# Kernel tuning notes

Hardware: AMD Instinct MI355X
Metric: run time of the kernel (lower is better)

## Reference

```python
import jax, jax.numpy as jnp
import numpy as np

E = 8          # num_experts
K = 2          # top-k experts per token
CAP_RATIO = 1.05


def setup_inputs() -> dict:
    key = jax.random.key(0)
    ks = jax.random.split(key, 4)
    B, S, D, H = 2, 2048, 1024, 4096
    x = jax.random.normal(ks[0], (B, S, D), jnp.float32)
    Wg = jax.random.normal(ks[1], (E, D), jnp.float32) * 0.02
    W1 = jax.random.normal(ks[2], (E, D, H), jnp.float32) * 0.02
    b1 = jnp.zeros((E, H), jnp.float32)
    W2 = jax.random.normal(ks[3], (E, H, D), jnp.float32) * 0.02
    b2 = jnp.zeros((E, D), jnp.float32)
    return {"x": x, "Wg": Wg, "W1": W1, "b1": b1, "W2": W2, "b2": b2}


def reference(x, Wg, W1, b1, W2, b2):
    # Eval-mode SparseMoE forward (no router noise, no aux-loss metrics).
    B, S, D = x.shape
    T = B * S
    xf = x.reshape(T, D)

    # --- router: softmax gates + top-k ---
    gates = jax.nn.softmax(xf @ Wg.T, axis=-1)          # [T, E]
    topw, topi = jax.lax.top_k(gates, K)                # [T, K]

    # --- capacity-limited dispatch (slot-major order, matching torch loop) ---
    C = int(round(K * T * CAP_RATIO / E))               # buffer capacity per expert
    e_ord = topi.T.reshape(-1)                          # [K*T] expert id per assignment
    tok_ord = jnp.tile(jnp.arange(T), K)                # [K*T] token id per assignment
    oh = jax.nn.one_hot(e_ord, E, dtype=jnp.int32)      # [K*T, E]
    cnt = jnp.take_along_axis(jnp.cumsum(oh, 0) - oh, e_ord[:, None], 1)[:, 0]
    within = cnt < C                                    # first C arrivals per expert accepted
    pos = jnp.where(within, cnt, C)                     # dropped tokens -> dummy slot C

    # scatter accepted tokens into per-expert buffers [E, C+1, D]
    x_disp = xf[tok_ord]
    buf = jnp.zeros((E, C + 1, D), xf.dtype).at[e_ord, pos].add(x_disp)[:, :C]

    # --- grouped expert MLP (Linear -> exact GELU -> Linear) ---
    h = jax.nn.gelu(jnp.einsum('ecd,edh->ech', buf, W1) + b1[:, None, :],
                    approximate=False)
    y = jnp.einsum('ech,ehd->ecd', h, W2) + b2[:, None, :]  # [E, C, D]

    # --- gather back and weighted combine ---
    y_ord = y[e_ord, jnp.minimum(pos, C - 1)] * within[:, None].astype(y.dtype)
    y_tk = y_ord.reshape(K, T, D).transpose(1, 0, 2)     # [T, K, D]
    cw = topw * within.reshape(K, T).T.astype(topw.dtype)
    out = jnp.einsum('tk,tkd->td', cw, y_tk)
    return out.reshape(B, S, D)
```

## Files before the change

kernel.cpp:

```cpp
#include <hip/hip_runtime.h>

typedef __attribute__((ext_vector_type(8))) __bf16 bf16x8;
typedef __attribute__((ext_vector_type(4))) float f32x4;

constexpr int T  = 4096;
constexpr int Dm = 1024;
constexpr int Hm = 4096;
constexpr int NE = 8;
constexpr int CAP = 1075;
constexpr int CP  = 1152;

static __device__ __forceinline__ unsigned short f2bf(float f) {
  unsigned int u = __float_as_uint(f);
  u += 0x7FFFu + ((u >> 16) & 1u);
  return (unsigned short)(u >> 16);
}

static __device__ __forceinline__ void gload_lds16(const void* g, void* l) {
  __builtin_amdgcn_global_load_lds(
      (const __attribute__((address_space(1))) void*)g,
      (__attribute__((address_space(3))) void*)l, 16, 0, 0);
}


static __device__ __forceinline__ void transpose_body(
    float (*tile)[33], const float* __restrict__ W, unsigned short* __restrict__ Wt,
    int Kd, int N, int e, int n0, int k0) {
  const float* src = W + ((long long)e * Kd + k0) * N + n0;
  const int tid = threadIdx.x;
  const int r = tid >> 3;
  const int c4 = (tid & 7) * 4;
#pragma unroll
  for (int hh = 0; hh < 2; ++hh) {
    float4 v = *(const float4*)(src + (long long)(r + 32 * hh) * N + c4);
    tile[r + 32 * hh][c4] = v.x; tile[r + 32 * hh][c4 + 1] = v.y;
    tile[r + 32 * hh][c4 + 2] = v.z; tile[r + 32 * hh][c4 + 3] = v.w;
  }
  __syncthreads();
  const int n = tid >> 4;
  const int k4 = (tid & 15) * 4;
  unsigned short* dst = Wt + ((long long)e * N + n0) * Kd + k0;
#pragma unroll
  for (int hh = 0; hh < 2; ++hh) {
    int nn = n + 16 * hh;
    ushort4 o;
    o.x = f2bf(tile[k4][nn]);     o.y = f2bf(tile[k4 + 1][nn]);
    o.z = f2bf(tile[k4 + 2][nn]); o.w = f2bf(tile[k4 + 3][nn]);
    *(ushort4*)(dst + (long long)nn * Kd + k4) = o;
  }
}

static __device__ __forceinline__ void router_body(
    const float* __restrict__ x, const float* __restrict__ Wg,
    int* __restrict__ topi, float* __restrict__ topw, int blk) {
  int t = blk * 4 + (threadIdx.x >> 6);
  int lane = threadIdx.x & 63;
  const float* xr = x + (size_t)t * Dm;
  float acc[NE];
#pragma unroll
  for (int e = 0; e < NE; ++e) acc[e] = 0.f;
  for (int i = lane * 4; i < Dm; i += 256) {
    float4 xv = *(const float4*)(xr + i);
#pragma unroll
    for (int e = 0; e < NE; ++e) {
      float4 wv = *(const float4*)(Wg + e * Dm + i);
      acc[e] += xv.x * wv.x + xv.y * wv.y + xv.z * wv.z + xv.w * wv.w;
    }
  }
#pragma unroll
  for (int off = 32; off > 0; off >>= 1) {
#pragma unroll
    for (int e = 0; e < NE; ++e) acc[e] += __shfl_xor(acc[e], off, 64);
  }
  if (lane == 0) {
    float mx = acc[0];
#pragma unroll
    for (int e = 1; e < NE; ++e) mx = fmaxf(mx, acc[e]);
    float g[NE];
    float s = 0.f;
#pragma unroll
    for (int e = 0; e < NE; ++e) { g[e] = expf(acc[e] - mx); s += g[e]; }
    int i0 = 0; float v0 = g[0];
#pragma unroll
    for (int e = 1; e < NE; ++e) if (g[e] > v0) { v0 = g[e]; i0 = e; }
    int i1 = -1; float v1 = -1e30f;
#pragma unroll
    for (int e = 0; e < NE; ++e) {
      if (e == i0) continue;
      if (g[e] > v1) { v1 = g[e]; i1 = e; }
    }
    float inv = 1.f / s;
    topi[t * 2] = i0; topi[t * 2 + 1] = i1;
    topw[t * 2] = v0 * inv; topw[t * 2 + 1] = v1 * inv;
  }
}

template <bool GELU, bool OUT_BF16>
static __device__ __forceinline__ void gemm_body(
    unsigned short* Alds, unsigned short* Blds,
    const unsigned short* __restrict__ A, const unsigned short* __restrict__ Bt,
    const float* __restrict__ bias, void* __restrict__ Out,
    int Kd, int N, int mb, int nb) {
  const unsigned short* Ab  = A  + (long long)mb * 128 * Kd;
  const unsigned short* Btb = Bt + (long long)nb * 128 * Kd;

  const int tid = threadIdx.x;
  const int lane = tid & 63;
  const int wid = tid >> 6;
  const int wr = (wid >> 1) * 64;
  const int wc = (wid & 1) * 64;
  const int l15 = lane & 15;
  const int khi = lane >> 4;
  const int swz = lane & 7;
  const int srow = lane >> 3;
  const int sslot = (lane & 7) ^ srow;

  f32x4 acc[4][4];
#pragma unroll
  for (int m = 0; m < 4; ++m)
#pragma unroll
    for (int n = 0; n < 4; ++n) acc[m][n] = (f32x4){0.f, 0.f, 0.f, 0.f};

  const int nK = Kd >> 6;
  for (int kt = 0; kt < nK; ++kt) {
    const int kb = kt << 6;
#pragma unroll
    for (int j = 0; j < 4; ++j) {
      const int c = wid * 4 + j;
      const long long rowg = 8 * c + srow;
      gload_lds16(Ab  + rowg * Kd + kb + sslot * 8, &Alds[c * 512]);
      gload_lds16(Btb + rowg * Kd + kb + sslot * 8, &Blds[c * 512]);
    }
    __syncthreads();
#pragma unroll
    for (int kk = 0; kk < 2; ++kk) {
      bf16x8 af[4], bfv[4];
#pragma unroll
      for (int m = 0; m < 4; ++m)
        af[m] = *(const bf16x8*)&Alds[(wr + m * 16 + l15) * 64 + (((kk * 4 + khi) ^ swz) << 3)];
#pragma unroll
      for (int n = 0; n < 4; ++n)
        bfv[n] = *(const bf16x8*)&Blds[(wc + n * 16 + l15) * 64 + (((kk * 4 + khi) ^ swz) << 3)];
#pragma unroll
      for (int m = 0; m < 4; ++m)
#pragma unroll
        for (int n = 0; n < 4; ++n)
          acc[m][n] = __builtin_amdgcn_mfma_f32_16x16x32_bf16(af[m], bfv[n], acc[m][n], 0, 0, 0);
    }
    __syncthreads();
  }

  const int crow = khi * 4;
#pragma unroll
  for (int m = 0; m < 4; ++m) {
#pragma unroll
    for (int n = 0; n < 4; ++n) {
      const long long col = (long long)nb * 128 + wc + n * 16 + l15;
      const float bvv = bias[nb * 128 + wc + n * 16 + l15];
#pragma unroll
      for (int j = 0; j < 4; ++j) {
        const long long row = (long long)mb * 128 + wr + m * 16 + crow + j;
        float v = acc[m][n][j] + bvv;
        if (GELU) v = 0.5f * v * (1.f + erff(v * 0.70710678118654752f));
        if (OUT_BF16)
          ((unsigned short*)Out)[row * N + col] = f2bf(v);
        else
          ((float*)Out)[row * N + col] = v;
      }
    }
  }
}


__global__ __launch_bounds__(256) void fused_pre_kernel(
    const float* __restrict__ x, const float* __restrict__ Wg,
    int* __restrict__ topi, float* __restrict__ topw,
    const float* __restrict__ W1, unsigned short* __restrict__ W1t,
    const float* __restrict__ W2, unsigned short* __restrict__ W2t,
    int nR, int nT) {
  __shared__ __align__(16) float tile[64][33];
  const int bid = blockIdx.x;
  if (bid < nR) {
    router_body(x, Wg, topi, topw, bid);
  } else if (bid < nR + nT) {
    int tb = bid - nR;
    int nb = tb % (Hm / 32);
    int rest = tb / (Hm / 32);
    int kb = rest % (Dm / 64);
    int e = rest / (Dm / 64);
    transpose_body(tile, W1, W1t, Dm, Hm, e, nb * 32, kb * 64);
  } else {
    int tb = bid - nR - nT;
    int nb = tb % (Dm / 32);
    int rest = tb / (Dm / 32);
    int kb = rest % (Hm / 64);
    int e = rest / (Hm / 64);
    transpose_body(tile, W2, W2t, Hm, Dm, e, nb * 32, kb * 64);
  }
}

__global__ __launch_bounds__(256) void transpose_kernel(
    const float* __restrict__ W, unsigned short* __restrict__ Wt, int Kd, int N) {
  __shared__ __align__(16) float tile[64][33];
  transpose_body(tile, W, Wt, Kd, N, blockIdx.z, blockIdx.x * 32, blockIdx.y * 64);
}

__global__ __launch_bounds__(1024) void dispatch_scan_kernel(
    const int* __restrict__ topi, int* __restrict__ pos, int* __restrict__ within) {
  __shared__ unsigned long long sc0[1024];
  __shared__ unsigned long long sc1[1024];
  const int tid = threadIdx.x;
  int myE[8];
  unsigned long long w0 = 0, w1 = 0;
#pragma unroll
  for (int j = 0; j < 8; ++j) {
    int a = tid * 8 + j;
    int k = a >> 12;
    int t = a & (T - 1);
    int e = topi[t * 2 + k];
    myE[j] = e;
    unsigned long long inc = 1ULL << (16 * (e & 3));
    if (e < 4) w0 += inc; else w1 += inc;
  }
  const unsigned long long l0 = w0, l1 = w1;
  sc0[tid] = w0; sc1[tid] = w1;
  __syncthreads();
  for (int off = 1; off < 1024; off <<= 1) {
    unsigned long long a0 = 0, a1 = 0;
    if (tid >= off) { a0 = sc0[tid - off]; a1 = sc1[tid - off]; }
    __syncthreads();
    w0 += a0; w1 += a1;
    sc0[tid] = w0; sc1[tid] = w1;
    __syncthreads();
  }
  unsigned long long e0 = w0 - l0, e1 = w1 - l1;
#pragma unroll
  for (int j = 0; j < 8; ++j) {
    int a = tid * 8 + j;
    int e = myE[j];
    int sh = 16 * (e & 3);
    int p;
    if (e < 4) { p = (int)((e0 >> sh) & 0xFFFF); e0 += 1ULL << sh; }
    else       { p = (int)((e1 >> sh) & 0xFFFF); e1 += 1ULL << sh; }
    pos[a] = p;
    within[a] = (p < CAP) ? 1 : 0;
  }
}

__global__ __launch_bounds__(256) void scatter_kernel(
    const float* __restrict__ x, const int* __restrict__ topi,
    const int* __restrict__ pos, const int* __restrict__ within,
    unsigned short* __restrict__ buf) {
  int a = blockIdx.x;
  if (!within[a]) return;
  int k = a >> 12, t = a & (T - 1);
  int e = topi[t * 2 + k];
  int p = pos[a];
  const float* src = x + (size_t)t * Dm;
  unsigned short* dst = buf + ((size_t)e * CP + p) * Dm;
  int i = threadIdx.x * 4;
  float4 v = *(const float4*)(src + i);
  ushort4 o;
  o.x = f2bf(v.x); o.y = f2bf(v.y); o.z = f2bf(v.z); o.w = f2bf(v.w);
  *(ushort4*)(dst + i) = o;
}

template <bool GELU, bool OUT_BF16>
__global__ __launch_bounds__(256) void gemm_bt_kernel(
    const unsigned short* __restrict__ Aall, const unsigned short* __restrict__ Btall,
    const float* __restrict__ biasAll, void* __restrict__ OutAll,
    int Kd, int N, long long sA, long long sB, long long sO, int sBias,
    int eb, int nM) {
  __shared__ __align__(16) char smem[32768];
  unsigned short* Alds = (unsigned short*)smem;
  unsigned short* Blds = (unsigned short*)(smem + 16384);
  const int lin = blockIdx.x;
  const int e = lin % eb;
  const int q = lin / eb;
  const int mb = q % nM;
  const int nb = q / nM;
  char* Out = (char*)OutAll + (long long)e * sO * (OUT_BF16 ? 2 : 4);
  gemm_body<GELU, OUT_BF16>(Alds, Blds,
      Aall + (long long)e * sA, Btall + (long long)e * sB,
      biasAll + (long long)e * sBias, (void*)Out, Kd, N, mb, nb);
}

__global__ __launch_bounds__(256) void combine_kernel(
    const float* __restrict__ y, const int* __restrict__ topi,
    const float* __restrict__ topw, const int* __restrict__ pos,
    const int* __restrict__ within, float* __restrict__ out) {
  int t = blockIdx.x;
  int i = threadIdx.x * 4;
  float4 r = {0.f, 0.f, 0.f, 0.f};
#pragma unroll
  for (int k = 0; k < 2; ++k) {
    int a = k * T + t;
    if (within[a]) {
      int e = topi[t * 2 + k];
      int p = pos[a];
      float w = topw[t * 2 + k];
      const float* yr = y + ((size_t)e * CP + p) * Dm;
      float4 v = *(const float4*)(yr + i);
      r.x += w * v.x; r.y += w * v.y; r.z += w * v.z; r.w += w * v.w;
    }
  }
  *(float4*)(out + (size_t)t * Dm + i) = r;
}

extern "C" void kernel_launch(void* const* d_in, const int* in_sizes, int n_in,
                              void* d_out, int out_size, void* d_ws, size_t ws_size,
                              hipStream_t stream) {
  const float* x  = (const float*)d_in[0];
  const float* Wg = (const float*)d_in[1];
  const float* W1 = (const float*)d_in[2];
  const float* b1 = (const float*)d_in[3];
  const float* W2 = (const float*)d_in[4];
  const float* b2 = (const float*)d_in[5];
  float* out = (float*)d_out;

  char* ws = (char*)d_ws;
  const size_t sz_h = (size_t)NE * CP * Hm * 2;
  const size_t sz_y = (size_t)NE * CP * Dm * 4;
  const size_t sz_w = (size_t)NE * Hm * Dm * 2;
  const size_t sz_small = (size_t)2 * T * 16;
  const size_t need_full = sz_h + sz_y + 2 * sz_w + sz_small;
  const size_t need_mid  = sz_h + sz_y + sz_w + sz_small;

  unsigned short* h = (unsigned short*)ws;
  char* yreg = ws + sz_h;
  unsigned short* buf = (unsigned short*)yreg;
  float* y = (float*)yreg;
  unsigned short* W1t = (unsigned short*)(ws + sz_h + sz_y);
  const bool full = (ws_size >= need_full);
  const bool mid  = (ws_size >= need_mid);
  unsigned short* W2t = full ? (W1t + sz_w / 2) : W1t;
  char* smallp = ws + sz_h + sz_y + (full ? 2 * sz_w : (mid ? sz_w : (size_t)2 * Hm * Dm * 2));
  int* topi   = (int*)smallp;
  float* topw = (float*)(topi + 2 * T);
  int* pos    = (int*)(topw + 2 * T);
  int* within = pos + 2 * T;

  const int nM = CP / 128;
  const int nR = T / 4;
  const int nT = (Hm / 32) * (Dm / 64) * NE;
  const int nGemm1 = NE * nM * (Hm / 128);
  const int nGemm2 = NE * nM * (Dm / 128);

  if (full) {
    fused_pre_kernel<<<nR + 2 * nT, 256, 0, stream>>>(
        x, Wg, topi, topw, W1, W1t, W2, W2t, nR, nT);
    dispatch_scan_kernel<<<1, 1024, 0, stream>>>(topi, pos, within);
    scatter_kernel<<<2 * T, 256, 0, stream>>>(x, topi, pos, within, buf);
    gemm_bt_kernel<true, true><<<nGemm1, 256, 0, stream>>>(
        buf, W1t, b1, (void*)h, Dm, Hm,
        (long long)CP * Dm, (long long)Hm * Dm, (long long)CP * Hm, Hm, NE, nM);
    gemm_bt_kernel<false, false><<<nGemm2, 256, 0, stream>>>(
        h, W2t, b2, (void*)y, Hm, Dm,
        (long long)CP * Hm, (long long)Dm * Hm, (long long)CP * Dm, Dm, NE, nM);
  } else if (mid) {
    fused_pre_kernel<<<nR + nT, 256, 0, stream>>>(
        x, Wg, topi, topw, W1, W1t, W2, W2t, nR, nT);
    dispatch_scan_kernel<<<1, 1024, 0, stream>>>(topi, pos, within);
    scatter_kernel<<<2 * T, 256, 0, stream>>>(x, topi, pos, within, buf);
    gemm_bt_kernel<true, true><<<nGemm1, 256, 0, stream>>>(
        buf, W1t, b1, (void*)h, Dm, Hm,
        (long long)CP * Dm, (long long)Hm * Dm, (long long)CP * Hm, Hm, NE, nM);
    transpose_kernel<<<dim3(Dm / 32, Hm / 64, NE), 256, 0, stream>>>(W2, W2t, Hm, Dm);
    gemm_bt_kernel<false, false><<<nGemm2, 256, 0, stream>>>(
        h, W2t, b2, (void*)y, Hm, Dm,
        (long long)CP * Hm, (long long)Dm * Hm, (long long)CP * Dm, Dm, NE, nM);
  } else {
    fused_pre_kernel<<<nR, 256, 0, stream>>>(
        x, Wg, topi, topw, W1, W1t, W2, W2t, nR, 0);
    dispatch_scan_kernel<<<1, 1024, 0, stream>>>(topi, pos, within);
    scatter_kernel<<<2 * T, 256, 0, stream>>>(x, topi, pos, within, buf);
    for (int e0 = 0; e0 < NE; e0 += 2) {
      transpose_kernel<<<dim3(Hm / 32, Dm / 64, 2), 256, 0, stream>>>(
          W1 + (size_t)e0 * Dm * Hm, W1t, Dm, Hm);
      gemm_bt_kernel<true, true><<<2 * nM * (Hm / 128), 256, 0, stream>>>(
          buf + (size_t)e0 * CP * Dm, W1t, b1 + (size_t)e0 * Hm,
          (void*)(h + (size_t)e0 * CP * Hm), Dm, Hm,
          (long long)CP * Dm, (long long)Hm * Dm, (long long)CP * Hm, Hm, 2, nM);
    }
    for (int e0 = 0; e0 < NE; e0 += 2) {
      transpose_kernel<<<dim3(Dm / 32, Hm / 64, 2), 256, 0, stream>>>(
          W2 + (size_t)e0 * Hm * Dm, W1t, Hm, Dm);
      gemm_bt_kernel<false, false><<<2 * nM * (Dm / 128), 256, 0, stream>>>(
          h + (size_t)e0 * CP * Hm, W1t, b2 + (size_t)e0 * Dm,
          (void*)(y + (size_t)e0 * CP * Dm), Hm, Dm,
          (long long)CP * Hm, (long long)Dm * Hm, (long long)CP * Dm, Dm, 2, nM);
    }
  }

  combine_kernel<<<T, 256, 0, stream>>>(y, topi, topw, pos, within, out);
}
```

Measured before the change: 347.0 us.

## Fuse combine into GEMM2 via atomic scatter and skip empty expert row tiles

Removes the separate combine kernel and the fp32 y buffer. GEMM2 now scatters gate-weighted results straight into the zeroed output with atomicAdd, using a per-slot inverse map of token and weight that the scatter kernel fills in. The output and inverse-map initialisation is folded into the fused pre-kernel. Both GEMMs read per-expert counts from the scan and exit early for row tiles beyond the filled capacity, trading the extra kernel and y traffic for float atomics and a non-deterministic summation order.

```diff
diff --git a/kernel.cpp b/kernel.cpp
--- a/kernel.cpp
+++ b/kernel.cpp
@@ -95,15 +95,10 @@
   }
 }
 
-template <bool GELU, bool OUT_BF16>
-static __device__ __forceinline__ void gemm_body(
+static __device__ __forceinline__ void gemm_mainloop(
     unsigned short* Alds, unsigned short* Blds,
-    const unsigned short* __restrict__ A, const unsigned short* __restrict__ Bt,
-    const float* __restrict__ bias, void* __restrict__ Out,
-    int Kd, int N, int mb, int nb) {
-  const unsigned short* Ab  = A  + (long long)mb * 128 * Kd;
-  const unsigned short* Btb = Bt + (long long)nb * 128 * Kd;
-
+    const unsigned short* __restrict__ Ab, const unsigned short* __restrict__ Btb,
+    int Kd, f32x4 (&acc)[4][4]) {
   const int tid = threadIdx.x;
   const int lane = tid & 63;
   const int wid = tid >> 6;
@@ -115,12 +110,6 @@
   const int srow = lane >> 3;
   const int sslot = (lane & 7) ^ srow;
 
-  f32x4 acc[4][4];
-#pragma unroll
-  for (int m = 0; m < 4; ++m)
-#pragma unroll
-    for (int n = 0; n < 4; ++n) acc[m][n] = (f32x4){0.f, 0.f, 0.f, 0.f};
-
   const int nK = Kd >> 6;
   for (int kt = 0; kt < nK; ++kt) {
     const int kb = kt << 6;
@@ -149,26 +138,6 @@
     }
     __syncthreads();
   }
-
-  const int crow = khi * 4;
-#pragma unroll
-  for (int m = 0; m < 4; ++m) {
-#pragma unroll
-    for (int n = 0; n < 4; ++n) {
-      const long long col = (long long)nb * 128 + wc + n * 16 + l15;
-      const float bvv = bias[nb * 128 + wc + n * 16 + l15];
-#pragma unroll
-      for (int j = 0; j < 4; ++j) {
-        const long long row = (long long)mb * 128 + wr + m * 16 + crow + j;
-        float v = acc[m][n][j] + bvv;
-        if (GELU) v = 0.5f * v * (1.f + erff(v * 0.70710678118654752f));
-        if (OUT_BF16)
-          ((unsigned short*)Out)[row * N + col] = f2bf(v);
-        else
-          ((float*)Out)[row * N + col] = v;
-      }
-    }
-  }
 }
 
 
@@ -177,25 +146,35 @@
     int* __restrict__ topi, float* __restrict__ topw,
     const float* __restrict__ W1, unsigned short* __restrict__ W1t,
     const float* __restrict__ W2, unsigned short* __restrict__ W2t,
-    int nR, int nT) {
+    float* __restrict__ out, int* __restrict__ inv_t,
+    int nI, int nR, int nT2, int nT1) {
   __shared__ __align__(16) float tile[64][33];
   const int bid = blockIdx.x;
-  if (bid < nR) {
-    router_body(x, Wg, topi, topw, bid);
-  } else if (bid < nR + nT) {
-    int tb = bid - nR;
+  if (bid < nI) {
+    const int nOut4 = (T * Dm) / 4;
+    int gid = bid * 256 + threadIdx.x;
+    if (gid < nOut4) {
+      ((float4*)out)[gid] = (float4){0.f, 0.f, 0.f, 0.f};
+    } else {
+      int r = gid - nOut4;
+      if (r < NE * CP) inv_t[r] = -1;
+    }
+  } else if (bid < nI + nR) {
+    router_body(x, Wg, topi, topw, bid - nI);
+  } else if (bid < nI + nR + nT2) {
+    int tb = bid - nI - nR;
+    int nb = tb % (Dm / 32);
+    int rest = tb / (Dm / 32);
+    int kb = rest % (Hm / 64);
+    int e = rest / (Hm / 64);
+    transpose_body(tile, W2, W2t, Hm, Dm, e, nb * 32, kb * 64);
+  } else {
+    int tb = bid - nI - nR - nT2;
     int nb = tb % (Hm / 32);
     int rest = tb / (Hm / 32);
     int kb = rest % (Dm / 64);
     int e = rest / (Dm / 64);
     transpose_body(tile, W1, W1t, Dm, Hm, e, nb * 32, kb * 64);
-  } else {
-    int tb = bid - nR - nT;
-    int nb = tb % (Dm / 32);
-    int rest = tb / (Dm / 32);
-    int kb = rest % (Hm / 64);
-    int e = rest / (Hm / 64);
-    transpose_body(tile, W2, W2t, Hm, Dm, e, nb * 32, kb * 64);
   }
 }
 
@@ -206,7 +185,8 @@
 }
 
 __global__ __launch_bounds__(1024) void dispatch_scan_kernel(
-    const int* __restrict__ topi, int* __restrict__ pos, int* __restrict__ within) {
+    const int* __restrict__ topi, int* __restrict__ pos, int* __restrict__ within,
+    int* __restrict__ cnt) {
   __shared__ unsigned long long sc0[1024];
   __shared__ unsigned long long sc1[1024];
   const int tid = threadIdx.x;
@@ -233,6 +213,13 @@
     sc0[tid] = w0; sc1[tid] = w1;
     __syncthreads();
   }
+  if (tid == 1023) {
+#pragma unroll
+    for (int e = 0; e < 4; ++e) {
+      cnt[e]     = (int)((w0 >> (16 * e)) & 0xFFFF);
+      cnt[e + 4] = (int)((w1 >> (16 * e)) & 0xFFFF);
+    }
+  }
   unsigned long long e0 = w0 - l0, e1 = w1 - l1;
 #pragma unroll
   for (int j = 0; j < 8; ++j) {
@@ -249,13 +236,18 @@
 
 __global__ __launch_bounds__(256) void scatter_kernel(
     const float* __restrict__ x, const int* __restrict__ topi,
-    const int* __restrict__ pos, const int* __restrict__ within,
-    unsigned short* __restrict__ buf) {
+    const float* __restrict__ topw, const int* __restrict__ pos,
+    const int* __restrict__ within, unsigned short* __restrict__ buf,
+    int* __restrict__ inv_t, float* __restrict__ inv_w) {
   int a = blockIdx.x;
   if (!within[a]) return;
   int k = a >> 12, t = a & (T - 1);
   int e = topi[t * 2 + k];
   int p = pos[a];
+  if (threadIdx.x == 0) {
+    inv_t[e * CP + p] = t;
+    inv_w[e * CP + p] = topw[t * 2 + k];
+  }
   const float* src = x + (size_t)t * Dm;
   unsigned short* dst = buf + ((size_t)e * CP + p) * Dm;
   int i = threadIdx.x * 4;
@@ -265,46 +257,109 @@
   *(ushort4*)(dst + i) = o;
 }
 
-template <bool GELU, bool OUT_BF16>
-__global__ __launch_bounds__(256) void gemm_bt_kernel(
-    const unsigned short* __restrict__ Aall, const unsigned short* __restrict__ Btall,
-    const float* __restrict__ biasAll, void* __restrict__ OutAll,
-    int Kd, int N, long long sA, long long sB, long long sO, int sBias,
-    int eb, int nM) {
+__global__ __launch_bounds__(256) void gemm1_kernel(
+    const unsigned short* __restrict__ buf, const unsigned short* __restrict__ W1t,
+    const float* __restrict__ b1, unsigned short* __restrict__ h,
+    const int* __restrict__ cnt) {
   __shared__ __align__(16) char smem[32768];
-  unsigned short* Alds = (unsigned short*)smem;
-  unsigned short* Blds = (unsigned short*)(smem + 16384);
-  const int lin = blockIdx.x;
-  const int e = lin % eb;
-  const int q = lin / eb;
-  const int mb = q % nM;
-  const int nb = q / nM;
-  char* Out = (char*)OutAll + (long long)e * sO * (OUT_BF16 ? 2 : 4);
-  gemm_body<GELU, OUT_BF16>(Alds, Blds,
-      Aall + (long long)e * sA, Btall + (long long)e * sB,
-      biasAll + (long long)e * sBias, (void*)Out, Kd, N, mb, nb);
-}
-
-__global__ __launch_bounds__(256) void combine_kernel(
-    const float* __restrict__ y, const int* __restrict__ topi,
-    const float* __restrict__ topw, const int* __restrict__ pos,
-    const int* __restrict__ within, float* __restrict__ out) {
-  int t = blockIdx.x;
-  int i = threadIdx.x * 4;
-  float4 r = {0.f, 0.f, 0.f, 0.f};
-#pragma unroll
-  for (int k = 0; k < 2; ++k) {
-    int a = k * T + t;
-    if (within[a]) {
-      int e = topi[t * 2 + k];
-      int p = pos[a];
-      float w = topw[t * 2 + k];
-      const float* yr = y + ((size_t)e * CP + p) * Dm;
-      float4 v = *(const float4*)(yr + i);
-      r.x += w * v.x; r.y += w * v.y; r.z += w * v.z; r.w += w * v.w;
-    }
-  }
-  *(float4*)(out + (size_t)t * Dm + i) = r;
+  const int e = blockIdx.x & 7;
+  const int q = blockIdx.x >> 3;
+  const int mb = q % (CP / 128);
+  const int nb = q / (CP / 128);
+  const int ce = min(cnt[e], CAP);
+  if (mb * 128 >= ce) return;
+
+  f32x4 acc[4][4];
+#pragma unroll
+  for (int m = 0; m < 4; ++m)
+#pragma unroll
+    for (int n = 0; n < 4; ++n) acc[m][n] = (f32x4){0.f, 0.f, 0.f, 0.f};
+
+  gemm_mainloop((unsigned short*)smem, (unsigned short*)(smem + 16384),
+                buf + ((long long)e * CP + mb * 128) * Dm,
+                W1t + ((long long)e * Hm + nb * 128) * Dm, Dm, acc);
+
+  const int lane = threadIdx.x & 63;
+  const int wid = threadIdx.x >> 6;
+  const int wr = (wid >> 1) * 64;
+  const int wc = (wid & 1) * 64;
+  const int l15 = lane & 15;
+  const int crow = (lane >> 4) * 4;
+  const float* bias = b1 + (size_t)e * Hm;
+  unsigned short* H = h + (size_t)e * CP * Hm;
+#pragma unroll
+  for (int m = 0; m < 4; ++m) {
+#pragma unroll
+    for (int n = 0; n < 4; ++n) {
+      const long long col = (long long)nb * 128 + wc + n * 16 + l15;
+      const float bvv = bias[col];
+#pragma unroll
+      for (int j = 0; j < 4; ++j) {
+        const long long row = (long long)mb * 128 + wr + m * 16 + crow + j;
+        float v = acc[m][n][j] + bvv;
+        v = 0.5f * v * (1.f + erff(v * 0.70710678118654752f));
+        H[row * Hm + col] = f2bf(v);
+      }
+    }
+  }
+}
+
+__global__ __launch_bounds__(256) void gemm2_kernel(
+    const unsigned short* __restrict__ h, const unsigned short* __restrict__ W2t,
+    const float* __restrict__ b2, const int* __restrict__ inv_t,
+    const float* __restrict__ inv_w, float* __restrict__ out,
+    const int* __restrict__ cnt) {
+  __shared__ __align__(16) char smem[32768];
+  const int e = blockIdx.x & 7;
+  const int q = blockIdx.x >> 3;
+  const int mb = q % (CP / 128);
+  const int nb = q / (CP / 128);
+  const int ce = min(cnt[e], CAP);
+  if (mb * 128 >= ce) return;
+
+  f32x4 acc[4][4];
+#pragma unroll
+  for (int m = 0; m < 4; ++m)
+#pragma unroll
+    for (int n = 0; n < 4; ++n) acc[m][n] = (f32x4){0.f, 0.f, 0.f, 0.f};
+
+  gemm_mainloop((unsigned short*)smem, (unsigned short*)(smem + 16384),
+                h + ((long long)e * CP + mb * 128) * Hm,
+                W2t + ((long long)e * Dm + nb * 128) * Hm, Hm, acc);
+
+  const int lane = threadIdx.x & 63;
+  const int wid = threadIdx.x >> 6;
+  const int wr = (wid >> 1) * 64;
+  const int wc = (wid & 1) * 64;
+  const int l15 = lane & 15;
+  const int crow = (lane >> 4) * 4;
+
+  int   tt[4][4];
+  float ww[4][4];
+#pragma unroll
+  for (int m = 0; m < 4; ++m)
+#pragma unroll
+    for (int j = 0; j < 4; ++j) {
+      const int row = mb * 128 + wr + m * 16 + crow + j;
+      tt[m][j] = inv_t[e * CP + row];
+      ww[m][j] = inv_w[e * CP + row];
+    }
+
+  const float* bias = b2 + (size_t)e * Dm;
+#pragma unroll
+  for (int m = 0; m < 4; ++m) {
+#pragma unroll
+    for (int n = 0; n < 4; ++n) {
+      const int col = nb * 128 + wc + n * 16 + l15;
+      const float bvv = bias[col];
+#pragma unroll
+      for (int j = 0; j < 4; ++j) {
+        float v = acc[m][n][j] + bvv;
+        if (tt[m][j] >= 0)
+          atomicAdd(out + (size_t)tt[m][j] * Dm + col, ww[m][j] * v);
+      }
+    }
+  }
 }
 
 extern "C" void kernel_launch(void* const* d_in, const int* in_sizes, int n_in,
@@ -319,78 +374,47 @@
   float* out = (float*)d_out;
 
   char* ws = (char*)d_ws;
-  const size_t sz_h = (size_t)NE * CP * Hm * 2;
-  const size_t sz_y = (size_t)NE * CP * Dm * 4;
-  const size_t sz_w = (size_t)NE * Hm * Dm * 2;
-  const size_t sz_small = (size_t)2 * T * 16;
-  const size_t need_full = sz_h + sz_y + 2 * sz_w + sz_small;
-  const size_t need_mid  = sz_h + sz_y + sz_w + sz_small;
-
-  unsigned short* h = (unsigned short*)ws;
-  char* yreg = ws + sz_h;
-  unsigned short* buf = (unsigned short*)yreg;
-  float* y = (float*)yreg;
-  unsigned short* W1t = (unsigned short*)(ws + sz_h + sz_y);
+  const size_t sz_h   = (size_t)NE * CP * Hm * 2;
+  const size_t sz_buf = (size_t)NE * CP * Dm * 2;
+  const size_t sz_w   = (size_t)NE * Hm * Dm * 2;
+  const size_t sz_small = (size_t)(NE * CP * 8 + 2 * T * 16 + 256);
+  const size_t need_full = sz_h + sz_buf + 2 * sz_w + sz_small;
+
+  unsigned short* h   = (unsigned short*)ws;
+  unsigned short* buf = (unsigned short*)(ws + sz_h);
+  unsigned short* W1t = (unsigned short*)(ws + sz_h + sz_buf);
   const bool full = (ws_size >= need_full);
-  const bool mid  = (ws_size >= need_mid);
   unsigned short* W2t = full ? (W1t + sz_w / 2) : W1t;
-  char* smallp = ws + sz_h + sz_y + (full ? 2 * sz_w : (mid ? sz_w : (size_t)2 * Hm * Dm * 2));
-  int* topi   = (int*)smallp;
-  float* topw = (float*)(topi + 2 * T);
-  int* pos    = (int*)(topw + 2 * T);
-  int* within = pos + 2 * T;
+  char* smallp = ws + sz_h + sz_buf + (full ? 2 * sz_w : sz_w);
+  int*   inv_t  = (int*)smallp;
+  float* inv_w  = (float*)(inv_t + NE * CP);
+  int*   topi   = (int*)(inv_w + NE * CP);
+  float* topw   = (float*)(topi + 2 * T);
+  int*   pos    = (int*)(topw + 2 * T);
+  int*   within = pos + 2 * T;
+  int*   cnt    = within + 2 * T;
 
   const int nM = CP / 128;
+  const int nI = (T * Dm / 4 + NE * CP + 255) / 256;
   const int nR = T / 4;
   const int nT = (Hm / 32) * (Dm / 64) * NE;
   const int nGemm1 = NE * nM * (Hm / 128);
   const int nGemm2 = NE * nM * (Dm / 128);
 
   if (full) {
-    fused_pre_kernel<<<nR + 2 * nT, 256, 0, stream>>>(
-        x, Wg, topi, topw, W1, W1t, W2, W2t, nR, nT);
-    dispatch_scan_kernel<<<1, 1024, 0, stream>>>(topi, pos, within);
-    scatter_kernel<<<2 * T, 256, 0, stream>>>(x, topi, pos, within, buf);
-    gemm_bt_kernel<true, true><<<nGemm1, 256, 0, stream>>>(
-        buf, W1t, b1, (void*)h, Dm, Hm,
-        (long long)CP * Dm, (long long)Hm * Dm, (long long)CP * Hm, Hm, NE, nM);
-    gemm_bt_kernel<false, false><<<nGemm2, 256, 0, stream>>>(
-        h, W2t, b2, (void*)y, Hm, Dm,
-        (long long)CP * Hm, (long long)Dm * Hm, (long long)CP * Dm, Dm, NE, nM);
-  } else if (mid) {
-    fused_pre_kernel<<<nR + nT, 256, 0, stream>>>(
-        x, Wg, topi, topw, W1, W1t, W2, W2t, nR, nT);
-    dispatch_scan_kernel<<<1, 1024, 0, stream>>>(topi, pos, within);
-    scatter_kernel<<<2 * T, 256, 0, stream>>>(x, topi, pos, within, buf);
-    gemm_bt_kernel<true, true><<<nGemm1, 256, 0, stream>>>(
-        buf, W1t, b1, (void*)h, Dm, Hm,
-        (long long)CP * Dm, (long long)Hm * Dm, (long long)CP * Hm, Hm, NE, nM);
+    fused_pre_kernel<<<nI + nR + 2 * nT, 256, 0, stream>>>(
+        x, Wg, topi, topw, W1, W1t, W2, W2t, out, inv_t, nI, nR, nT, nT);
+    dispatch_scan_kernel<<<1, 1024, 0, stream>>>(topi, pos, within, cnt);
+    scatter_kernel<<<2 * T, 256, 0, stream>>>(x, topi, topw, pos, within, buf, inv_t, inv_w);
+    gemm1_kernel<<<nGemm1, 256, 0, stream>>>(buf, W1t, b1, h, cnt);
+    gemm2_kernel<<<nGemm2, 256, 0, stream>>>(h, W2t, b2, inv_t, inv_w, out, cnt);
+  } else {
+    fused_pre_kernel<<<nI + nR + nT, 256, 0, stream>>>(
+        x, Wg, topi, topw, W1, W1t, W2, W2t, out, inv_t, nI, nR, 0, nT);
+    dispatch_scan_kernel<<<1, 1024, 0, stream>>>(topi, pos, within, cnt);
+    scatter_kernel<<<2 * T, 256, 0, stream>>>(x, topi, topw, pos, within, buf, inv_t, inv_w);
+    gemm1_kernel<<<nGemm1, 256, 0, stream>>>(buf, W1t, b1, h, cnt);
     transpose_kernel<<<dim3(Dm / 32, Hm / 64, NE), 256, 0, stream>>>(W2, W2t, Hm, Dm);
-    gemm_bt_kernel<false, false><<<nGemm2, 256, 0, stream>>>(
-        h, W2t, b2, (void*)y, Hm, Dm,
-        (long long)CP * Hm, (long long)Dm * Hm, (long long)CP * Dm, Dm, NE, nM);
-  } else {
-    fused_pre_kernel<<<nR, 256, 0, stream>>>(
-        x, Wg, topi, topw, W1, W1t, W2, W2t, nR, 0);
-    dispatch_scan_kernel<<<1, 1024, 0, stream>>>(topi, pos, within);
-    scatter_kernel<<<2 * T, 256, 0, stream>>>(x, topi, pos, within, buf);
-    for (int e0 = 0; e0 < NE; e0 += 2) {
-      transpose_kernel<<<dim3(Hm / 32, Dm / 64, 2), 256, 0, stream>>>(
-          W1 + (size_t)e0 * Dm * Hm, W1t, Dm, Hm);
-      gemm_bt_kernel<true, true><<<2 * nM * (Hm / 128), 256, 0, stream>>>(
-          buf + (size_t)e0 * CP * Dm, W1t, b1 + (size_t)e0 * Hm,
-          (void*)(h + (size_t)e0 * CP * Hm), Dm, Hm,
-          (long long)CP * Dm, (long long)Hm * Dm, (long long)CP * Hm, Hm, 2, nM);
-    }
-    for (int e0 = 0; e0 < NE; e0 += 2) {
-      transpose_kernel<<<dim3(Dm / 32, Hm / 64, 2), 256, 0, stream>>>(
-          W2 + (size_t)e0 * Hm * Dm, W1t, Hm, Dm);
-      gemm_bt_kernel<false, false><<<2 * nM * (Dm / 128), 256, 0, stream>>>(
-          h + (size_t)e0 * CP * Hm, W1t, b2 + (size_t)e0 * Dm,
-          (void*)(y + (size_t)e0 * CP * Dm), Hm, Dm,
-          (long long)CP * Hm, (long long)Dm * Hm, (long long)CP * Dm, Dm, 2, nM);
-    }
-  }
-
-  combine_kernel<<<T, 256, 0, stream>>>(y, topi, topw, pos, within, out);
-}
+    gemm2_kernel<<<nGemm2, 256, 0, stream>>>(h, W2t, b2, inv_t, inv_w, out, cnt);
+  }
+}
```

New measurement: 443.4 us. 1.28x slower.
